# Kernel tuning notes

Hardware: AMD Instinct MI355X
Metric: run time of the kernel (lower is better)

## Reference

```python
import jax, jax.numpy as jnp
import numpy as np

B = 2048   # batch
C = 64     # EEG channels (num_eegch)
T = 125    # time samples -> pool5 -> 25 -> (p=5, 5)
H = 8      # num_heads
L = 6      # num_layers
D = 16     # num_projected_features
QK = 8     # qkv_len
P = 5      # tokens before cls
EPS = 1e-5


def setup_inputs() -> dict:
    key = jax.random.key(0)
    ks = iter(jax.random.split(key, 64))

    def nrm(shape, s=0.05):
        return jax.random.normal(next(ks), shape, jnp.float32) * s

    return {
        "x": jax.random.normal(next(ks), (B, 1, C, T), jnp.float32),
        "conv_t_w": nrm((8, 1, 1, 63)),
        "conv_t_b": nrm((8,)),
        "bn1_g": 1.0 + nrm((8,)),
        "bn1_b": nrm((8,)),
        "bn1_m": nrm((8,)),
        "bn1_v": 1.0 + 0.1 * jax.random.uniform(next(ks), (8,), jnp.float32),
        "conv_s_w": nrm((16, 1, C, 1)),
        "conv_s_b": nrm((16,)),
        "bn2_g": 1.0 + nrm((16,)),
        "bn2_b": nrm((16,)),
        "bn2_m": nrm((16,)),
        "bn2_v": 1.0 + 0.1 * jax.random.uniform(next(ks), (16,), jnp.float32),
        "proj_w": nrm((D, 16 * 5)),
        "proj_b": nrm((D,)),
        "cls_token": nrm((1, 1, D), 1.0),
        "pe": nrm((1, P + 1, D), 1.0),
        "qkv_w": nrm((L, 3 * H * QK, D)),
        "qkv_b": nrm((L, 3 * H * QK)),
        "out_w": nrm((L, D, H * QK)),
        "out_b": nrm((L, D)),
        "ln1_g": jnp.ones((L, D), jnp.float32),
        "ln1_b": jnp.zeros((L, D), jnp.float32),
        "ln2_g": jnp.ones((L, D), jnp.float32),
        "ln2_b": jnp.zeros((L, D), jnp.float32),
        "mlp_w1": nrm((L, 2 * D, D)),
        "mlp_b1": nrm((L, 2 * D)),
        "mlp_w2": nrm((L, D, 2 * D)),
        "mlp_b2": nrm((L, D)),
        "head_ln_g": jnp.ones((D,), jnp.float32),
        "head_ln_b": jnp.zeros((D,), jnp.float32),
        "head_w": nrm((2, D)),
        "head_b": nrm((2,)),
    }


def _bn(z, g, b, m, v):
    s = (g * jax.lax.rsqrt(v + EPS))[None, :, None, None]
    return (z - m[None, :, None, None]) * s + b[None, :, None, None]


def _ln(z, g, b):
    m = z.mean(-1, keepdims=True)
    var = jnp.mean((z - m) ** 2, -1, keepdims=True)
    return (z - m) * jax.lax.rsqrt(var + EPS) * g + b


def _forward(x, conv_t_w, conv_t_b, bn1_g, bn1_b, bn1_m, bn1_v,
             conv_s_w, conv_s_b, bn2_g, bn2_b, bn2_m, bn2_v,
             proj_w, proj_b, cls_token, pe,
             qkv_w, qkv_b, out_w, out_b, ln1_g, ln1_b, ln2_g, ln2_b,
             mlp_w1, mlp_b1, mlp_w2, mlp_b2,
             head_ln_g, head_ln_b, head_w, head_b):
    b = x.shape[0]
    dn = ('NCHW', 'OIHW', 'NCHW')
    # temporal conv, 'same' padding on width (kernel 63 -> pad 31/31)
    y = jax.lax.conv_general_dilated(x, conv_t_w, (1, 1), [(0, 0), (31, 31)], dimension_numbers=dn)
    y = _bn(y + conv_t_b[None, :, None, None], bn1_g, bn1_b, bn1_m, bn1_v)
    # grouped spatial conv collapses the EEG-channel axis
    y = jax.lax.conv_general_dilated(y, conv_s_w, (1, 1), 'VALID', dimension_numbers=dn, feature_group_count=8)
    y = _bn(y + conv_s_b[None, :, None, None], bn2_g, bn2_b, bn2_m, bn2_v)
    y = jax.nn.elu(y)                              # (b,16,1,125)
    y = y.reshape(b, 16, 1, T // 5, 5).mean(-1)    # avg_pool2d (1,5) -> (b,16,1,25)
    # dropout: identity at inference
    y = y.reshape(b, 16, 1, P, 5)
    y = jnp.swapaxes(y, 3, 4)
    tok = jnp.swapaxes(y.reshape(b, 16 * 5, P), 1, 2)   # (b,5,80)
    tok = tok @ proj_w.T + proj_b                       # (b,5,16)
    z = jnp.concatenate([jnp.broadcast_to(cls_token, (b, 1, D)), tok], axis=1) + pe  # (b,6,16)
    scale = QK ** -0.5
    for i in range(L):
        h1 = _ln(z, ln1_g[i], ln1_b[i])
        qkv = h1 @ qkv_w[i].T + qkv_b[i]                # (b,6,3*H*QK)
        q, k, v = jnp.split(qkv, 3, axis=-1)
        q = q.reshape(b, P + 1, H, QK).transpose(0, 2, 1, 3)
        k = k.reshape(b, P + 1, H, QK).transpose(0, 2, 1, 3)
        v = v.reshape(b, P + 1, H, QK).transpose(0, 2, 1, 3)
        att = jax.nn.softmax(jnp.einsum('bhsd,bhtd->bhst', q, k) * scale, axis=-1)
        o = jnp.einsum('bhst,bhtd->bhsd', att, v).transpose(0, 2, 1, 3).reshape(b, P + 1, H * QK)
        z = o @ out_w[i].T + out_b[i] + z
        h2 = _ln(z, ln2_g[i], ln2_b[i])
        m = jax.nn.gelu(h2 @ mlp_w1[i].T + mlp_b1[i], approximate=False) @ mlp_w2[i].T + mlp_b2[i]
        z = m + z
    cls = _ln(z[:, 0, :], head_ln_g, head_ln_b)
    return jax.nn.softmax(cls @ head_w.T + head_b, axis=-1)


def reference(x, conv_t_w, conv_t_b, bn1_g, bn1_b, bn1_m, bn1_v,
              conv_s_w, conv_s_b, bn2_g, bn2_b, bn2_m, bn2_v,
              proj_w, proj_b, cls_token, pe,
              qkv_w, qkv_b, out_w, out_b, ln1_g, ln1_b, ln2_g, ln2_b,
              mlp_w1, mlp_b1, mlp_w2, mlp_b2,
              head_ln_g, head_ln_b, head_w, head_b):
    return _forward(x, conv_t_w, conv_t_b, bn1_g, bn1_b, bn1_m, bn1_v,
                    conv_s_w, conv_s_b, bn2_g, bn2_b, bn2_m, bn2_v,
                    proj_w, proj_b, cls_token, pe,
                    qkv_w, qkv_b, out_w, out_b, ln1_g, ln1_b, ln2_g, ln2_b,
                    mlp_w1, mlp_b1, mlp_w2, mlp_b2,
                    head_ln_g, head_ln_b, head_w, head_b)
```

## Files before the change

### kernel.cpp

```cpp
#include <hip/hip_runtime.h>

#define WAVE_SYNC() do { asm volatile("" ::: "memory"); \
                         __builtin_amdgcn_wave_barrier(); \
                         asm volatile("" ::: "memory"); } while (0)

__device__ __forceinline__ float ln_norm16(float z, float g, float bb) {
    float s = z, q = z * z;
    #pragma unroll
    for (int off = 8; off >= 1; off >>= 1) {
        s += __shfl_xor(s, off, 16);
        q += __shfl_xor(q, off, 16);
    }
    float mean = s * 0.0625f;
    float var  = q * 0.0625f - mean * mean;
    return (z - mean) * rsqrtf(var + 1e-5f) * g + bb;
}

__device__ __forceinline__ float gelu_exact(float a) {
    float xa = fabsf(a) * 0.70710678118654752f;
    float tt = 1.f / (1.f + 0.3275911f * xa);
    float poly = tt * (0.254829592f + tt * (-0.284496736f + tt * (1.421413741f
               + tt * (-1.453152027f + tt * 1.061405429f))));
    float erfv = 1.f - poly * __expf(-xa * xa);
    erfv = a >= 0.f ? erfv : -erfv;
    return 0.5f * a * (1.f + erfv);
}

__device__ __forceinline__ float dot16(const float* h, float4 w0, float4 w1,
                                       float4 w2, float4 w3) {
    return h[0]*w0.x + h[1]*w0.y + h[2]*w0.z + h[3]*w0.w
         + h[4]*w1.x + h[5]*w1.y + h[6]*w1.z + h[7]*w1.w
         + h[8]*w2.x + h[9]*w2.y + h[10]*w2.z + h[11]*w2.w
         + h[12]*w3.x + h[13]*w3.y + h[14]*w3.z + h[15]*w3.w;
}

#define F_XS  0
#define F_PL  3168
#define F_TOT 3616

extern "C" __global__ __launch_bounds__(64, 2)
void eegnet_frontend(
    const float* __restrict__ x,
    const float* __restrict__ conv_t_w, const float* __restrict__ conv_t_b,
    const float* __restrict__ bn1_g, const float* __restrict__ bn1_b,
    const float* __restrict__ bn1_m, const float* __restrict__ bn1_v,
    const float* __restrict__ conv_s_w, const float* __restrict__ conv_s_b,
    const float* __restrict__ bn2_g, const float* __restrict__ bn2_b,
    const float* __restrict__ bn2_m, const float* __restrict__ bn2_v,
    const float* __restrict__ proj_w, const float* __restrict__ proj_b,
    float* __restrict__ tokws)
{
    __shared__ __align__(16) float sm[F_TOT];
    const int b    = blockIdx.x;
    const int lane = threadIdx.x;

    for (int i = lane; i < 16 * 73; i += 64) {
        int row = i / 73, k = i - row * 73;
        int off = (k < 32) ? k : (k + 125);
        sm[F_XS + row * 198 + off] = 0.f;
    }

    {
        const float* xb = x + (size_t)b * 8000;
        const int l2 = min(lane, 60);
        float a0[16], a1[16];
        #pragma unroll
        for (int o = 0; o < 16; ++o) { a0[o] = 0.f; a1[o] = 0.f; }
        #pragma unroll 16
        for (int c = 0; c < 64; ++c) {
            float xv0 = xb[c * 125 + lane];
            float xv1 = xb[c * 125 + 64 + l2];
            #pragma unroll
            for (int o = 0; o < 16; ++o) {
                float w = conv_s_w[o * 64 + c];
                a0[o] += w * xv0;
                a1[o] += w * xv1;
            }
        }
        #pragma unroll
        for (int o = 0; o < 16; ++o) {
            sm[F_XS + o * 198 + 32 + lane] = a0[o];
            if (lane < 61) sm[F_XS + o * 198 + 96 + lane] = a1[o];
        }
    }

    const int oo = lane & 15, qg = lane >> 4, gg = oo >> 1;
    float sa, cc;
    {
        float s1 = bn1_g[gg] * rsqrtf(bn1_v[gg] + 1e-5f);
        float b1 = (conv_t_b[gg] - bn1_m[gg]) * s1 + bn1_b[gg];
        float s2 = bn2_g[oo] * rsqrtf(bn2_v[oo] + 1e-5f);
        float ssum = 0.f;
        const float4* csw = reinterpret_cast<const float4*>(conv_s_w + oo * 64);
        #pragma unroll
        for (int i = 0; i < 16; ++i) {
            float4 v = csw[i];
            ssum += v.x + v.y + v.z + v.w;
        }
        sa = s1 * s2;
        cc = (b1 * ssum + conv_s_b[oo] - bn2_m[oo]) * s2 + bn2_b[oo];
    }
    float wt[63];
    #pragma unroll
    for (int k = 0; k < 63; ++k) wt[k] = conv_t_w[gg * 63 + k];

    WAVE_SYNC();

    #pragma unroll 1
    for (int jj = 0; jj < 7; ++jj) {
        int j  = qg * 7 + jj;
        int jc = min(j, 24);
        int base = F_XS + oo * 198 + 5 * jc + 1;
        float acc5[5] = {0.f, 0.f, 0.f, 0.f, 0.f};
        #pragma unroll
        for (int m = 0; m < 67; ++m) {
            float xv = sm[base + m];
            #pragma unroll
            for (int u = 0; u < 5; ++u)
                if (u <= m && m - u <= 62) acc5[u] += wt[m - u] * xv;
        }
        float psum = 0.f;
        #pragma unroll
        for (int u = 0; u < 5; ++u) {
            float v = acc5[u] * sa + cc;
            psum += (v > 0.f) ? v : (__expf(v) - 1.f);
        }
        if (j == jc) sm[F_PL + oo * 28 + j] = psum * 0.2f;
    }

    WAVE_SYNC();

    #pragma unroll
    for (int pass = 0; pass < 2; ++pass) {
        int oi = (pass == 0) ? lane : (64 + lane);
        int p = oi >> 4, dd = oi & 15;
        int pc = min(p, 4);
        bool act = (pass == 0) || (lane < 16);
        float acc = proj_b[dd];
        const float4* wp = reinterpret_cast<const float4*>(proj_w + dd * 80);
        #pragma unroll
        for (int i = 0; i < 20; ++i) {
            float4 w4 = wp[i];
            acc += w4.x * sm[F_PL + ((4*i+0)/5) * 28 + pc * 5 + ((4*i+0)%5)];
            acc += w4.y * sm[F_PL + ((4*i+1)/5) * 28 + pc * 5 + ((4*i+1)%5)];
            acc += w4.z * sm[F_PL + ((4*i+2)/5) * 28 + pc * 5 + ((4*i+2)%5)];
            acc += w4.w * sm[F_PL + ((4*i+3)/5) * 28 + pc * 5 + ((4*i+3)%5)];
        }
        if (act) tokws[b * 80 + pc * 16 + dd] = acc;
    }
}

#define WQKV 0
#define BQKV 3840
#define WOUT 4032
#define BOUT 5120
#define WM1  5136
#define BM1  5776
#define WM2  5808
#define BM2  6384
#define LN1G 6400
#define LN1B 6416
#define LN2G 6432
#define LN2B 6448
#define WEND 6464
#define SSTR 1568
#define SH1  0
#define SQKV 128
#define SMHS 1312
#define T_TOT (WEND + 4*SSTR)

extern "C" __global__ __launch_bounds__(256, 2)
void eegnet_transformer(
    const float* __restrict__ cls_token, const float* __restrict__ pe,
    const float* __restrict__ qkv_w, const float* __restrict__ qkv_b,
    const float* __restrict__ out_w, const float* __restrict__ out_b,
    const float* __restrict__ ln1_g, const float* __restrict__ ln1_b,
    const float* __restrict__ ln2_g, const float* __restrict__ ln2_b,
    const float* __restrict__ mlp_w1, const float* __restrict__ mlp_b1,
    const float* __restrict__ mlp_w2, const float* __restrict__ mlp_b2,
    const float* __restrict__ head_ln_g, const float* __restrict__ head_ln_b,
    const float* __restrict__ head_w, const float* __restrict__ head_b,
    const float* __restrict__ tokws, float* __restrict__ out)
{
    __shared__ __align__(16) float sm[T_TOT];
    const int tid = threadIdx.x;
    const int ss  = tid >> 7;
    const int u   = tid & 127;
    const int sA  = blockIdx.x * 4 + ss * 2;
    const int d16 = u & 15, qg = u >> 4;
    const int t6c = min(qg, 5);
    const int wav = u >> 6, al = u & 63;
    const int sbA = WEND + (ss * 2    ) * SSTR;
    const int sbB = WEND + (ss * 2 + 1) * SSTR;

    float zA, zB;
    {
        float peV = pe[t6c * 16 + d16];
        if (t6c == 0) {
            float cv = cls_token[d16];
            zA = cv + peV; zB = cv + peV;
        } else {
            zA = tokws[(sA    ) * 80 + (t6c - 1) * 16 + d16] + peV;
            zB = tokws[(sA + 1) * 80 + (t6c - 1) * 16 + d16] + peV;
        }
    }

    #pragma unroll 1
    for (int li = 0; li < 6; ++li) {
        __syncthreads();

        {
            const float4* s1 = reinterpret_cast<const float4*>(qkv_w + li * 3072);
            #pragma unroll
            for (int it = 0; it < 3; ++it) {
                int i = tid + it * 256;
                float4 v = s1[i];
                int j = i >> 2, k = (i & 3) << 2;
                *reinterpret_cast<float4*>(&sm[WQKV + j * 20 + k]) = v;
            }
            {
                float4 v = reinterpret_cast<const float4*>(out_w + li * 1024)[tid];
                int j = tid >> 4, k = (tid & 15) << 2;
                *reinterpret_cast<float4*>(&sm[WOUT + j * 68 + k]) = v;
            }
            if (tid < 128) {
                float4 v = reinterpret_cast<const float4*>(mlp_w1 + li * 512)[tid];
                int j = tid >> 2, k = (tid & 3) << 2;
                *reinterpret_cast<float4*>(&sm[WM1 + j * 20 + k]) = v;
            } else {
                int i = tid - 128;
                float4 v = reinterpret_cast<const float4*>(mlp_w2 + li * 512)[i];
                int j = i >> 3, k = (i & 7) << 2;
                *reinterpret_cast<float4*>(&sm[WM2 + j * 36 + k]) = v;
            }
            if (tid < 192) sm[BQKV + tid] = qkv_b[li * 192 + tid];
            else if (tid < 208) sm[BOUT + tid - 192] = out_b[li * 16 + tid - 192];
            else if (tid < 240) sm[BM1 + tid - 208]  = mlp_b1[li * 32 + tid - 208];
            else               sm[BM2 + tid - 240]  = mlp_b2[li * 16 + tid - 240];
            if (tid >= 64 && tid < 80)        sm[LN1G + tid - 64]  = ln1_g[li * 16 + tid - 64];
            else if (tid >= 80 && tid < 96)   sm[LN1B + tid - 80]  = ln1_b[li * 16 + tid - 80];
            else if (tid >= 96 && tid < 112)  sm[LN2G + tid - 96]  = ln2_g[li * 16 + tid - 96];
            else if (tid >= 112 && tid < 128) sm[LN2B + tid - 112] = ln2_b[li * 16 + tid - 112];
        }
        __syncthreads();

        {
            float g = sm[LN1G + d16], bb = sm[LN1B + d16];
            sm[sbA + SH1 + t6c * 20 + d16] = ln_norm16(zA, g, bb);
            sm[sbB + SH1 + t6c * 20 + d16] = ln_norm16(zB, g, bb);
        }
        WAVE_SYNC();

        float hrA[16], hrB[16];
        {
            const float4* pA = reinterpret_cast<const float4*>(&sm[sbA + SH1 + t6c * 20]);
            const float4* pB = reinterpret_cast<const float4*>(&sm[sbB + SH1 + t6c * 20]);
            #pragma unroll
            for (int i = 0; i < 4; ++i) {
                float4 va = pA[i], vb = pB[i];
                hrA[4*i+0]=va.x; hrA[4*i+1]=va.y; hrA[4*i+2]=va.z; hrA[4*i+3]=va.w;
                hrB[4*i+0]=vb.x; hrB[4*i+1]=vb.y; hrB[4*i+2]=vb.z; hrB[4*i+3]=vb.w;
            }
        }

        #pragma unroll 2
        for (int r = 0; r < 12; ++r) {
            int j = d16 + 16 * r;
            const float4* wp = reinterpret_cast<const float4*>(&sm[WQKV + j * 20]);
            float4 w0 = wp[0], w1_ = wp[1], w2_ = wp[2], w3_ = wp[3];
            float bb = sm[BQKV + j];
            sm[sbA + SQKV + t6c * 196 + j] = bb + dot16(hrA, w0, w1_, w2_, w3_);
            sm[sbB + SQKV + t6c * 196 + j] = bb + dot16(hrB, w0, w1_, w2_, w3_);
        }
        __syncthreads();

        {
            bool act = (wav == 0) ? (al < 32) : (al < 16);
            if (act) {
                int h  = al & 7;
                int qs = (wav == 0) ? (al >> 3) : 4 + (al >> 3);
                const int qoffA = sbA + SQKV + qs * 196 + h * 8;
                const int qoffB = sbB + SQKV + qs * 196 + h * 8;
                const float4* qpA = reinterpret_cast<const float4*>(&sm[qoffA]);
                const float4* qpB = reinterpret_cast<const float4*>(&sm[qoffB]);
                float4 qA0 = qpA[0], qA1 = qpA[1], qB0 = qpB[0], qB1 = qpB[1];
                float scA[6], scB[6];
                #pragma unroll
                for (int t = 0; t < 6; ++t) {
                    const float4* kA = reinterpret_cast<const float4*>(&sm[sbA + SQKV + t * 196 + 64 + h * 8]);
                    const float4* kB = reinterpret_cast<const float4*>(&sm[sbB + SQKV + t * 196 + 64 + h * 8]);
                    float4 a0 = kA[0], a1 = kA[1], b0 = kB[0], b1 = kB[1];
                    scA[t] = (qA0.x*a0.x + qA0.y*a0.y + qA0.z*a0.z + qA0.w*a0.w
                            + qA1.x*a1.x + qA1.y*a1.y + qA1.z*a1.z + qA1.w*a1.w)
                            * 0.35355339059327373f;
                    scB[t] = (qB0.x*b0.x + qB0.y*b0.y + qB0.z*b0.z + qB0.w*b0.w
                            + qB1.x*b1.x + qB1.y*b1.y + qB1.z*b1.z + qB1.w*b1.w)
                            * 0.35355339059327373f;
                }
                float mxA = scA[0], mxB = scB[0];
                #pragma unroll
                for (int t = 1; t < 6; ++t) { mxA = fmaxf(mxA, scA[t]); mxB = fmaxf(mxB, scB[t]); }
                float suA = 0.f, suB = 0.f;
                #pragma unroll
                for (int t = 0; t < 6; ++t) {
                    scA[t] = __expf(scA[t] - mxA); suA += scA[t];
                    scB[t] = __expf(scB[t] - mxB); suB += scB[t];
                }
                float ivA = 1.f / suA, ivB = 1.f / suB;
                float oA[8] = {0,0,0,0,0,0,0,0}, oB[8] = {0,0,0,0,0,0,0,0};
                #pragma unroll
                for (int t = 0; t < 6; ++t) {
                    const float4* vA = reinterpret_cast<const float4*>(&sm[sbA + SQKV + t * 196 + 128 + h * 8]);
                    const float4* vB = reinterpret_cast<const float4*>(&sm[sbB + SQKV + t * 196 + 128 + h * 8]);
                    float4 a0 = vA[0], a1 = vA[1], b0 = vB[0], b1 = vB[1];
                    float aa = scA[t] * ivA, ab = scB[t] * ivB;
                    oA[0]+=aa*a0.x; oA[1]+=aa*a0.y; oA[2]+=aa*a0.z; oA[3]+=aa*a0.w;
                    oA[4]+=aa*a1.x; oA[5]+=aa*a1.y; oA[6]+=aa*a1.z; oA[7]+=aa*a1.w;
                    oB[0]+=ab*b0.x; oB[1]+=ab*b0.y; oB[2]+=ab*b0.z; oB[3]+=ab*b0.w;
                    oB[4]+=ab*b1.x; oB[5]+=ab*b1.y; oB[6]+=ab*b1.z; oB[7]+=ab*b1.w;
                }
                *reinterpret_cast<float4*>(&sm[qoffA    ]) = float4{oA[0],oA[1],oA[2],oA[3]};
                *reinterpret_cast<float4*>(&sm[qoffA + 4]) = float4{oA[4],oA[5],oA[6],oA[7]};
                *reinterpret_cast<float4*>(&sm[qoffB    ]) = float4{oB[0],oB[1],oB[2],oB[3]};
                *reinterpret_cast<float4*>(&sm[qoffB + 4]) = float4{oB[4],oB[5],oB[6],oB[7]};
            }
        }
        WAVE_SYNC();

        {
            const float4* wop = reinterpret_cast<const float4*>(&sm[WOUT + d16 * 68]);
            const float4* oaA = reinterpret_cast<const float4*>(&sm[sbA + SQKV + t6c * 196]);
            const float4* oaB = reinterpret_cast<const float4*>(&sm[sbB + SQKV + t6c * 196]);
            float bb = sm[BOUT + d16];
            float aA = bb, aB = bb;
            #pragma unroll 4
            for (int i = 0; i < 16; ++i) {
                float4 w = wop[i];
                float4 va = oaA[i], vb = oaB[i];
                aA += va.x*w.x + va.y*w.y + va.z*w.z + va.w*w.w;
                aB += vb.x*w.x + vb.y*w.y + vb.z*w.z + vb.w*w.w;
            }
            zA += aA; zB += aB;
        }

        {
            float g = sm[LN2G + d16], bb = sm[LN2B + d16];
            sm[sbA + SH1 + t6c * 20 + d16] = ln_norm16(zA, g, bb);
            sm[sbB + SH1 + t6c * 20 + d16] = ln_norm16(zB, g, bb);
        }
        WAVE_SYNC();
        {
            const float4* pA = reinterpret_cast<const float4*>(&sm[sbA + SH1 + t6c * 20]);
            const float4* pB = reinterpret_cast<const float4*>(&sm[sbB + SH1 + t6c * 20]);
            #pragma unroll
            for (int i = 0; i < 4; ++i) {
                float4 va = pA[i], vb = pB[i];
                hrA[4*i+0]=va.x; hrA[4*i+1]=va.y; hrA[4*i+2]=va.z; hrA[4*i+3]=va.w;
                hrB[4*i+0]=vb.x; hrB[4*i+1]=vb.y; hrB[4*i+2]=vb.z; hrB[4*i+3]=vb.w;
            }
        }

        #pragma unroll
        for (int r = 0; r < 2; ++r) {
            int uu = d16 + 16 * r;
            const float4* wp = reinterpret_cast<const float4*>(&sm[WM1 + uu * 20]);
            float4 w0 = wp[0], w1_ = wp[1], w2_ = wp[2], w3_ = wp[3];
            float bb = sm[BM1 + uu];
            float aA = bb + dot16(hrA, w0, w1_, w2_, w3_);
            float aB = bb + dot16(hrB, w0, w1_, w2_, w3_);
            sm[sbA + SMHS + t6c * 36 + uu] = gelu_exact(aA);
            sm[sbB + SMHS + t6c * 36 + uu] = gelu_exact(aB);
        }
        WAVE_SYNC();

        {
            const float4* wp = reinterpret_cast<const float4*>(&sm[WM2 + d16 * 36]);
            const float4* mA = reinterpret_cast<const float4*>(&sm[sbA + SMHS + t6c * 36]);
            const float4* mB = reinterpret_cast<const float4*>(&sm[sbB + SMHS + t6c * 36]);
            float bb = sm[BM2 + d16];
            float aA = bb, aB = bb;
            #pragma unroll
            for (int i = 0; i < 8; ++i) {
                float4 w = wp[i];
                float4 va = mA[i], vb = mB[i];
                aA += va.x*w.x + va.y*w.y + va.z*w.z + va.w*w.w;
                aB += vb.x*w.x + vb.y*w.y + vb.z*w.z + vb.w*w.w;
            }
            zA += aA; zB += aB;
        }
    }

    if (u < 16) {
        float g = head_ln_g[d16], bb = head_ln_b[d16];
        float w0 = head_w[d16], w1 = head_w[16 + d16];
        float cvA = ln_norm16(zA, g, bb);
        float cvB = ln_norm16(zB, g, bb);
        float pA0 = cvA * w0, pA1 = cvA * w1;
        float pB0 = cvB * w0, pB1 = cvB * w1;
        #pragma unroll
        for (int off = 8; off >= 1; off >>= 1) {
            pA0 += __shfl_xor(pA0, off, 16);
            pA1 += __shfl_xor(pA1, off, 16);
            pB0 += __shfl_xor(pB0, off, 16);
            pB1 += __shfl_xor(pB1, off, 16);
        }
        if (u == 0) {
            float hb0 = head_b[0], hb1 = head_b[1];
            {
                float l0 = pA0 + hb0, l1 = pA1 + hb1;
                float mx = fmaxf(l0, l1);
                float e0 = __expf(l0 - mx), e1 = __expf(l1 - mx);
                float inv = 1.f / (e0 + e1);
                out[sA * 2 + 0] = e0 * inv;
                out[sA * 2 + 1] = e1 * inv;
            }
            {
                float l0 = pB0 + hb0, l1 = pB1 + hb1;
                float mx = fmaxf(l0, l1);
                float e0 = __expf(l0 - mx), e1 = __expf(l1 - mx);
                float inv = 1.f / (e0 + e1);
                out[(sA + 1) * 2 + 0] = e0 * inv;
                out[(sA + 1) * 2 + 1] = e1 * inv;
            }
        }
    }
}

extern "C" void kernel_launch(void* const* d_in, const int* in_sizes, int n_in,
                              void* d_out, int out_size, void* d_ws, size_t ws_size,
                              hipStream_t stream) {
    (void)n_in; (void)ws_size; (void)out_size;
    const float* a0  = (const float*)d_in[0];
    const float* a1  = (const float*)d_in[1];
    const float* a2  = (const float*)d_in[2];
    const float* a3  = (const float*)d_in[3];
    const float* a4  = (const float*)d_in[4];
    const float* a5  = (const float*)d_in[5];
    const float* a6  = (const float*)d_in[6];
    const float* a7  = (const float*)d_in[7];
    const float* a8  = (const float*)d_in[8];
    const float* a9  = (const float*)d_in[9];
    const float* a10 = (const float*)d_in[10];
    const float* a11 = (const float*)d_in[11];
    const float* a12 = (const float*)d_in[12];
    const float* a13 = (const float*)d_in[13];
    const float* a14 = (const float*)d_in[14];
    const float* a15 = (const float*)d_in[15];
    const float* a16 = (const float*)d_in[16];
    const float* a17 = (const float*)d_in[17];
    const float* a18 = (const float*)d_in[18];
    const float* a19 = (const float*)d_in[19];
    const float* a20 = (const float*)d_in[20];
    const float* a21 = (const float*)d_in[21];
    const float* a22 = (const float*)d_in[22];
    const float* a23 = (const float*)d_in[23];
    const float* a24 = (const float*)d_in[24];
    const float* a25 = (const float*)d_in[25];
    const float* a26 = (const float*)d_in[26];
    const float* a27 = (const float*)d_in[27];
    const float* a28 = (const float*)d_in[28];
    const float* a29 = (const float*)d_in[29];
    const float* a30 = (const float*)d_in[30];
    const float* a31 = (const float*)d_in[31];
    const float* a32 = (const float*)d_in[32];

    int Bn = in_sizes[0] / (64 * 125);
    float* tokws = (float*)d_ws;

    eegnet_frontend<<<Bn, 64, 0, stream>>>(
        a0, a1, a2, a3, a4, a5, a6, a7, a8, a9, a10, a11, a12, a13, a14, tokws);

    eegnet_transformer<<<Bn / 4, 256, 0, stream>>>(
        a15, a16, a17, a18, a19, a20, a21, a22, a23, a24, a25, a26, a27, a28,
        a29, a30, a31, a32, tokws, (float*)d_out);
}
```

Before: 233.0 us.

## Store transformer weights and activations in fp16 shared memory and use packed dot2

```diff
diff --git a/kernel.cpp b/kernel.cpp
--- a/kernel.cpp
+++ b/kernel.cpp
@@ -3,6 +3,37 @@
 #define WAVE_SYNC() do { asm volatile("" ::: "memory"); \
                          __builtin_amdgcn_wave_barrier(); \
                          asm volatile("" ::: "memory"); } while (0)
+
+typedef _Float16 h2 __attribute__((ext_vector_type(2)));
+typedef _Float16 h4 __attribute__((ext_vector_type(4)));
+typedef _Float16 h8 __attribute__((ext_vector_type(8)));
+
+__device__ __forceinline__ float fdot2(h2 a, h2 b, float c) {
+#if defined(__has_builtin)
+#if __has_builtin(__builtin_amdgcn_fdot2)
+    return __builtin_amdgcn_fdot2(a, b, c, false);
+#else
+    return (float)a[0]*(float)b[0] + (float)a[1]*(float)b[1] + c;
+#endif
+#else
+    return (float)a[0]*(float)b[0] + (float)a[1]*(float)b[1] + c;
+#endif
+}
+
+__device__ __forceinline__ float dot8h(h8 a, h8 b, float c) {
+    float s = c;
+    #pragma unroll
+    for (int i = 0; i < 4; ++i) {
+        h2 x = {a[2*i], a[2*i+1]};
+        h2 y = {b[2*i], b[2*i+1]};
+        s = fdot2(x, y, s);
+    }
+    return s;
+}
+
+__device__ __forceinline__ float dot16h(h8 a0, h8 a1, h8 b0, h8 b1, float c) {
+    return dot8h(a1, b1, dot8h(a0, b0, c));
+}
 
 __device__ __forceinline__ float ln_norm16(float z, float g, float bb) {
     float s = z, q = z * z;
@@ -24,14 +55,6 @@
     float erfv = 1.f - poly * __expf(-xa * xa);
     erfv = a >= 0.f ? erfv : -erfv;
     return 0.5f * a * (1.f + erfv);
-}
-
-__device__ __forceinline__ float dot16(const float* h, float4 w0, float4 w1,
-                                       float4 w2, float4 w3) {
-    return h[0]*w0.x + h[1]*w0.y + h[2]*w0.z + h[3]*w0.w
-         + h[4]*w1.x + h[5]*w1.y + h[6]*w1.z + h[7]*w1.w
-         + h[8]*w2.x + h[9]*w2.y + h[10]*w2.z + h[11]*w2.w
-         + h[12]*w3.x + h[13]*w3.y + h[14]*w3.z + h[15]*w3.w;
 }
 
 #define F_XS  0
@@ -106,7 +129,7 @@
 
     WAVE_SYNC();
 
-    #pragma unroll 1
+    #pragma unroll 2
     for (int jj = 0; jj < 7; ++jj) {
         int j  = qg * 7 + jj;
         int jc = min(j, 24);
@@ -150,24 +173,24 @@
     }
 }
 
-#define WQKV 0
-#define BQKV 3840
-#define WOUT 4032
-#define BOUT 5120
-#define WM1  5136
-#define BM1  5776
-#define WM2  5808
-#define BM2  6384
-#define LN1G 6400
-#define LN1B 6416
-#define LN2G 6432
-#define LN2B 6448
-#define WEND 6464
-#define SSTR 1568
-#define SH1  0
-#define SQKV 128
-#define SMHS 1312
-#define T_TOT (WEND + 4*SSTR)
+#define WQKVH 0
+#define WOUTH 4608
+#define WM1H  5760
+#define WM2H  6528
+#define BQKVF 3584
+#define BOUTF 3776
+#define BM1F  3792
+#define BM2F  3824
+#define LN1GF 3840
+#define LN1BF 3856
+#define LN2GF 3872
+#define LN2BF 3888
+#define SCR0  7808
+#define SSTRH 1584
+#define SH1H  0
+#define SQKVH 144
+#define SMHSH 1344
+#define T_BYTES 28288
 
 extern "C" __global__ __launch_bounds__(256, 2)
 void eegnet_transformer(
@@ -182,7 +205,10 @@
     const float* __restrict__ head_w, const float* __restrict__ head_b,
     const float* __restrict__ tokws, float* __restrict__ out)
 {
-    __shared__ __align__(16) float sm[T_TOT];
+    __shared__ __align__(16) unsigned char smb[T_BYTES];
+    float*    smf = reinterpret_cast<float*>(smb);
+    _Float16* smh = reinterpret_cast<_Float16*>(smb);
+
     const int tid = threadIdx.x;
     const int ss  = tid >> 7;
     const int u   = tid & 127;
@@ -190,8 +216,8 @@
     const int d16 = u & 15, qg = u >> 4;
     const int t6c = min(qg, 5);
     const int wav = u >> 6, al = u & 63;
-    const int sbA = WEND + (ss * 2    ) * SSTR;
-    const int sbB = WEND + (ss * 2 + 1) * SSTR;
+    const int sbA = SCR0 + (ss * 2    ) * SSTRH;
+    const int sbB = SCR0 + (ss * 2 + 1) * SSTRH;
 
     float zA, zB;
     {
@@ -216,61 +242,58 @@
                 int i = tid + it * 256;
                 float4 v = s1[i];
                 int j = i >> 2, k = (i & 3) << 2;
-                *reinterpret_cast<float4*>(&sm[WQKV + j * 20 + k]) = v;
+                h4 hv = {(_Float16)v.x, (_Float16)v.y, (_Float16)v.z, (_Float16)v.w};
+                *reinterpret_cast<h4*>(&smh[WQKVH + j * 24 + k]) = hv;
             }
             {
                 float4 v = reinterpret_cast<const float4*>(out_w + li * 1024)[tid];
                 int j = tid >> 4, k = (tid & 15) << 2;
-                *reinterpret_cast<float4*>(&sm[WOUT + j * 68 + k]) = v;
+                h4 hv = {(_Float16)v.x, (_Float16)v.y, (_Float16)v.z, (_Float16)v.w};
+                *reinterpret_cast<h4*>(&smh[WOUTH + j * 72 + k]) = hv;
             }
             if (tid < 128) {
                 float4 v = reinterpret_cast<const float4*>(mlp_w1 + li * 512)[tid];
                 int j = tid >> 2, k = (tid & 3) << 2;
-                *reinterpret_cast<float4*>(&sm[WM1 + j * 20 + k]) = v;
+                h4 hv = {(_Float16)v.x, (_Float16)v.y, (_Float16)v.z, (_Float16)v.w};
+                *reinterpret_cast<h4*>(&smh[WM1H + j * 24 + k]) = hv;
             } else {
                 int i = tid - 128;
                 float4 v = reinterpret_cast<const float4*>(mlp_w2 + li * 512)[i];
                 int j = i >> 3, k = (i & 7) << 2;
-                *reinterpret_cast<float4*>(&sm[WM2 + j * 36 + k]) = v;
-            }
-            if (tid < 192) sm[BQKV + tid] = qkv_b[li * 192 + tid];
-            else if (tid < 208) sm[BOUT + tid - 192] = out_b[li * 16 + tid - 192];
-            else if (tid < 240) sm[BM1 + tid - 208]  = mlp_b1[li * 32 + tid - 208];
-            else               sm[BM2 + tid - 240]  = mlp_b2[li * 16 + tid - 240];
-            if (tid >= 64 && tid < 80)        sm[LN1G + tid - 64]  = ln1_g[li * 16 + tid - 64];
-            else if (tid >= 80 && tid < 96)   sm[LN1B + tid - 80]  = ln1_b[li * 16 + tid - 80];
-            else if (tid >= 96 && tid < 112)  sm[LN2G + tid - 96]  = ln2_g[li * 16 + tid - 96];
-            else if (tid >= 112 && tid < 128) sm[LN2B + tid - 112] = ln2_b[li * 16 + tid - 112];
+                h4 hv = {(_Float16)v.x, (_Float16)v.y, (_Float16)v.z, (_Float16)v.w};
+                *reinterpret_cast<h4*>(&smh[WM2H + j * 40 + k]) = hv;
+            }
+            if (tid < 192) smf[BQKVF + tid] = qkv_b[li * 192 + tid];
+            else if (tid < 208) smf[BOUTF + tid - 192] = out_b[li * 16 + tid - 192];
+            else if (tid < 240) smf[BM1F + tid - 208]  = mlp_b1[li * 32 + tid - 208];
+            else               smf[BM2F + tid - 240]  = mlp_b2[li * 16 + tid - 240];
+            if (tid >= 64 && tid < 80)        smf[LN1GF + tid - 64]  = ln1_g[li * 16 + tid - 64];
+            else if (tid >= 80 && tid < 96)   smf[LN1BF + tid - 80]  = ln1_b[li * 16 + tid - 80];
+            else if (tid >= 96 && tid < 112)  smf[LN2GF + tid - 96]  = ln2_g[li * 16 + tid - 96];
+            else if (tid >= 112 && tid < 128) smf[LN2BF + tid - 112] = ln2_b[li * 16 + tid - 112];
         }
         __syncthreads();
 
         {
-            float g = sm[LN1G + d16], bb = sm[LN1B + d16];
-            sm[sbA + SH1 + t6c * 20 + d16] = ln_norm16(zA, g, bb);
-            sm[sbB + SH1 + t6c * 20 + d16] = ln_norm16(zB, g, bb);
+            float g = smf[LN1GF + d16], bb = smf[LN1BF + d16];
+            smh[sbA + SH1H + t6c * 24 + d16] = (_Float16)ln_norm16(zA, g, bb);
+            smh[sbB + SH1H + t6c * 24 + d16] = (_Float16)ln_norm16(zB, g, bb);
         }
         WAVE_SYNC();
 
-        float hrA[16], hrB[16];
-        {
-            const float4* pA = reinterpret_cast<const float4*>(&sm[sbA + SH1 + t6c * 20]);
-            const float4* pB = reinterpret_cast<const float4*>(&sm[sbB + SH1 + t6c * 20]);
-            #pragma unroll
-            for (int i = 0; i < 4; ++i) {
-                float4 va = pA[i], vb = pB[i];
-                hrA[4*i+0]=va.x; hrA[4*i+1]=va.y; hrA[4*i+2]=va.z; hrA[4*i+3]=va.w;
-                hrB[4*i+0]=vb.x; hrB[4*i+1]=vb.y; hrB[4*i+2]=vb.z; hrB[4*i+3]=vb.w;
-            }
-        }
+        h8 hA0 = *reinterpret_cast<const h8*>(&smh[sbA + SH1H + t6c * 24]);
+        h8 hA1 = *reinterpret_cast<const h8*>(&smh[sbA + SH1H + t6c * 24 + 8]);
+        h8 hB0 = *reinterpret_cast<const h8*>(&smh[sbB + SH1H + t6c * 24]);
+        h8 hB1 = *reinterpret_cast<const h8*>(&smh[sbB + SH1H + t6c * 24 + 8]);
 
         #pragma unroll 2
         for (int r = 0; r < 12; ++r) {
             int j = d16 + 16 * r;
-            const float4* wp = reinterpret_cast<const float4*>(&sm[WQKV + j * 20]);
-            float4 w0 = wp[0], w1_ = wp[1], w2_ = wp[2], w3_ = wp[3];
-            float bb = sm[BQKV + j];
-            sm[sbA + SQKV + t6c * 196 + j] = bb + dot16(hrA, w0, w1_, w2_, w3_);
-            sm[sbB + SQKV + t6c * 196 + j] = bb + dot16(hrB, w0, w1_, w2_, w3_);
+            h8 w0 = *reinterpret_cast<const h8*>(&smh[WQKVH + j * 24]);
+            h8 w1 = *reinterpret_cast<const h8*>(&smh[WQKVH + j * 24 + 8]);
+            float bb = smf[BQKVF + j];
+            smh[sbA + SQKVH + t6c * 200 + j] = (_Float16)dot16h(hA0, hA1, w0, w1, bb);
+            smh[sbB + SQKVH + t6c * 200 + j] = (_Float16)dot16h(hB0, hB1, w0, w1, bb);
         }
         __syncthreads();
 
@@ -279,23 +302,17 @@
             if (act) {
                 int h  = al & 7;
                 int qs = (wav == 0) ? (al >> 3) : 4 + (al >> 3);
-                const int qoffA = sbA + SQKV + qs * 196 + h * 8;
-                const int qoffB = sbB + SQKV + qs * 196 + h * 8;
-                const float4* qpA = reinterpret_cast<const float4*>(&sm[qoffA]);
-                const float4* qpB = reinterpret_cast<const float4*>(&sm[qoffB]);
-                float4 qA0 = qpA[0], qA1 = qpA[1], qB0 = qpB[0], qB1 = qpB[1];
+                const int qoffA = sbA + SQKVH + qs * 200 + h * 8;
+                const int qoffB = sbB + SQKVH + qs * 200 + h * 8;
+                h8 qA = *reinterpret_cast<const h8*>(&smh[qoffA]);
+                h8 qB = *reinterpret_cast<const h8*>(&smh[qoffB]);
                 float scA[6], scB[6];
                 #pragma unroll
                 for (int t = 0; t < 6; ++t) {
-                    const float4* kA = reinterpret_cast<const float4*>(&sm[sbA + SQKV + t * 196 + 64 + h * 8]);
-                    const float4* kB = reinterpret_cast<const float4*>(&sm[sbB + SQKV + t * 196 + 64 + h * 8]);
-                    float4 a0 = kA[0], a1 = kA[1], b0 = kB[0], b1 = kB[1];
-                    scA[t] = (qA0.x*a0.x + qA0.y*a0.y + qA0.z*a0.z + qA0.w*a0.w
-                            + qA1.x*a1.x + qA1.y*a1.y + qA1.z*a1.z + qA1.w*a1.w)
-                            * 0.35355339059327373f;
-                    scB[t] = (qB0.x*b0.x + qB0.y*b0.y + qB0.z*b0.z + qB0.w*b0.w
-                            + qB1.x*b1.x + qB1.y*b1.y + qB1.z*b1.z + qB1.w*b1.w)
-                            * 0.35355339059327373f;
+                    h8 kA = *reinterpret_cast<const h8*>(&smh[sbA + SQKVH + t * 200 + 64 + h * 8]);
+                    h8 kB = *reinterpret_cast<const h8*>(&smh[sbB + SQKVH + t * 200 + 64 + h * 8]);
+                    scA[t] = dot8h(qA, kA, 0.f) * 0.35355339059327373f;
+                    scB[t] = dot8h(qB, kB, 0.f) * 0.35355339059327373f;
                 }
                 float mxA = scA[0], mxB = scB[0];
                 #pragma unroll
@@ -307,84 +324,82 @@
                     scB[t] = __expf(scB[t] - mxB); suB += scB[t];
                 }
                 float ivA = 1.f / suA, ivB = 1.f / suB;
-                float oA[8] = {0,0,0,0,0,0,0,0}, oB[8] = {0,0,0,0,0,0,0,0};
+                h2 oA[4], oB[4];
+                #pragma unroll
+                for (int k2 = 0; k2 < 4; ++k2) { oA[k2] = h2{0, 0}; oB[k2] = h2{0, 0}; }
                 #pragma unroll
                 for (int t = 0; t < 6; ++t) {
-                    const float4* vA = reinterpret_cast<const float4*>(&sm[sbA + SQKV + t * 196 + 128 + h * 8]);
-                    const float4* vB = reinterpret_cast<const float4*>(&sm[sbB + SQKV + t * 196 + 128 + h * 8]);
-                    float4 a0 = vA[0], a1 = vA[1], b0 = vB[0], b1 = vB[1];
-                    float aa = scA[t] * ivA, ab = scB[t] * ivB;
-                    oA[0]+=aa*a0.x; oA[1]+=aa*a0.y; oA[2]+=aa*a0.z; oA[3]+=aa*a0.w;
-                    oA[4]+=aa*a1.x; oA[5]+=aa*a1.y; oA[6]+=aa*a1.z; oA[7]+=aa*a1.w;
-                    oB[0]+=ab*b0.x; oB[1]+=ab*b0.y; oB[2]+=ab*b0.z; oB[3]+=ab*b0.w;
-                    oB[4]+=ab*b1.x; oB[5]+=ab*b1.y; oB[6]+=ab*b1.z; oB[7]+=ab*b1.w;
+                    h8 vA = *reinterpret_cast<const h8*>(&smh[sbA + SQKVH + t * 200 + 128 + h * 8]);
+                    h8 vB = *reinterpret_cast<const h8*>(&smh[sbB + SQKVH + t * 200 + 128 + h * 8]);
+                    _Float16 aa = (_Float16)(scA[t] * ivA);
+                    _Float16 ab = (_Float16)(scB[t] * ivB);
+                    h2 av = {aa, aa}, bv = {ab, ab};
+                    #pragma unroll
+                    for (int k2 = 0; k2 < 4; ++k2) {
+                        h2 va = {vA[2*k2], vA[2*k2+1]};
+                        h2 vb = {vB[2*k2], vB[2*k2+1]};
+                        oA[k2] += av * va;
+                        oB[k2] += bv * vb;
+                    }
                 }
-                *reinterpret_cast<float4*>(&sm[qoffA    ]) = float4{oA[0],oA[1],oA[2],oA[3]};
-                *reinterpret_cast<float4*>(&sm[qoffA + 4]) = float4{oA[4],oA[5],oA[6],oA[7]};
-                *reinterpret_cast<float4*>(&sm[qoffB    ]) = float4{oB[0],oB[1],oB[2],oB[3]};
-                *reinterpret_cast<float4*>(&sm[qoffB + 4]) = float4{oB[4],oB[5],oB[6],oB[7]};
+                h8 stA, stB;
+                #pragma unroll
+                for (int k2 = 0; k2 < 4; ++k2) {
+                    stA[2*k2] = oA[k2][0]; stA[2*k2+1] = oA[k2][1];
+                    stB[2*k2] = oB[k2][0]; stB[2*k2+1] = oB[k2][1];
+                }
+                *reinterpret_cast<h8*>(&smh[qoffA]) = stA;
+                *reinterpret_cast<h8*>(&smh[qoffB]) = stB;
             }
         }
         WAVE_SYNC();
 
         {
-            const float4* wop = reinterpret_cast<const float4*>(&sm[WOUT + d16 * 68]);
-            const float4* oaA = reinterpret_cast<const float4*>(&sm[sbA + SQKV + t6c * 196]);
-            const float4* oaB = reinterpret_cast<const float4*>(&sm[sbB + SQKV + t6c * 196]);
-            float bb = sm[BOUT + d16];
-            float aA = bb, aB = bb;
-            #pragma unroll 4
-            for (int i = 0; i < 16; ++i) {
-                float4 w = wop[i];
-                float4 va = oaA[i], vb = oaB[i];
-                aA += va.x*w.x + va.y*w.y + va.z*w.z + va.w*w.w;
-                aB += vb.x*w.x + vb.y*w.y + vb.z*w.z + vb.w*w.w;
+            float aA = smf[BOUTF + d16], aB = aA;
+            #pragma unroll
+            for (int i = 0; i < 8; ++i) {
+                h8 w  = *reinterpret_cast<const h8*>(&smh[WOUTH + d16 * 72 + 8 * i]);
+                h8 va = *reinterpret_cast<const h8*>(&smh[sbA + SQKVH + t6c * 200 + 8 * i]);
+                h8 vb = *reinterpret_cast<const h8*>(&smh[sbB + SQKVH + t6c * 200 + 8 * i]);
+                aA = dot8h(va, w, aA);
+                aB = dot8h(vb, w, aB);
             }
             zA += aA; zB += aB;
         }
 
         {
-            float g = sm[LN2G + d16], bb = sm[LN2B + d16];
-            sm[sbA + SH1 + t6c * 20 + d16] = ln_norm16(zA, g, bb);
-            sm[sbB + SH1 + t6c * 20 + d16] = ln_norm16(zB, g, bb);
+            float g = smf[LN2GF + d16], bb = smf[LN2BF + d16];
+            smh[sbA + SH1H + t6c * 24 + d16] = (_Float16)ln_norm16(zA, g, bb);
+            smh[sbB + SH1H + t6c * 24 + d16] = (_Float16)ln_norm16(zB, g, bb);
         }
         WAVE_SYNC();
-        {
-            const float4* pA = reinterpret_cast<const float4*>(&sm[sbA + SH1 + t6c * 20]);
-            const float4* pB = reinterpret_cast<const float4*>(&sm[sbB + SH1 + t6c * 20]);
+        hA0 = *reinterpret_cast<const h8*>(&smh[sbA + SH1H + t6c * 24]);
+        hA1 = *reinterpret_cast<const h8*>(&smh[sbA + SH1H + t6c * 24 + 8]);
+        hB0 = *reinterpret_cast<const h8*>(&smh[sbB + SH1H + t6c * 24]);
+        hB1 = *reinterpret_cast<const h8*>(&smh[sbB + SH1H + t6c * 24 + 8]);
+
+        #pragma unroll
+        for (int r = 0; r < 2; ++r) {
+            int uu = d16 + 16 * r;
+            h8 w0 = *reinterpret_cast<const h8*>(&smh[WM1H + uu * 24]);
+            h8 w1 = *reinterpret_cast<const h8*>(&smh[WM1H + uu * 24 + 8]);
+            float bb = smf[BM1F + uu];
+            float aA = dot16h(hA0, hA1, w0, w1, bb);
+            float aB = dot16h(hB0, hB1, w0, w1, bb);
+            smh[sbA + SMHSH + t6c * 40 + uu] = (_Float16)gelu_exact(aA);
+            smh[sbB + SMHSH + t6c * 40 + uu] = (_Float16)gelu_exact(aB);
+        }
+        WAVE_SYNC();
+
+        {
+            float aA = smf[BM2F + d16], aB = aA;
             #pragma unroll
             for (int i = 0; i < 4; ++i) {
-                float4 va = pA[i], vb = pB[i];
-                hrA[4*i+0]=va.x; hrA[4*i+1]=va.y; hrA[4*i+2]=va.z; hrA[4*i+3]=va.w;
-                hrB[4*i+0]=vb.x; hrB[4*i+1]=vb.y; hrB[4*i+2]=vb.z; hrB[4*i+3]=vb.w;
-            }
-        }
-
-        #pragma unroll
-        for (int r = 0; r < 2; ++r) {
-            int uu = d16 + 16 * r;
-            const float4* wp = reinterpret_cast<const float4*>(&sm[WM1 + uu * 20]);
-            float4 w0 = wp[0], w1_ = wp[1], w2_ = wp[2], w3_ = wp[3];
-            float bb = sm[BM1 + uu];
-            float aA = bb + dot16(hrA, w0, w1_, w2_, w3_);
-            float aB = bb + dot16(hrB, w0, w1_, w2_, w3_);
-            sm[sbA + SMHS + t6c * 36 + uu] = gelu_exact(aA);
-            sm[sbB + SMHS + t6c * 36 + uu] = gelu_exact(aB);
-        }
-        WAVE_SYNC();
-
-        {
-            const float4* wp = reinterpret_cast<const float4*>(&sm[WM2 + d16 * 36]);
-            const float4* mA = reinterpret_cast<const float4*>(&sm[sbA + SMHS + t6c * 36]);
-            const float4* mB = reinterpret_cast<const float4*>(&sm[sbB + SMHS + t6c * 36]);
-            float bb = sm[BM2 + d16];
-            float aA = bb, aB = bb;
-            #pragma unroll
-            for (int i = 0; i < 8; ++i) {
-                float4 w = wp[i];
-                float4 va = mA[i], vb = mB[i];
-                aA += va.x*w.x + va.y*w.y + va.z*w.z + va.w*w.w;
-                aB += vb.x*w.x + vb.y*w.y + vb.z*w.z + vb.w*w.w;
+                h8 w  = *reinterpret_cast<const h8*>(&smh[WM2H + d16 * 40 + 8 * i]);
+                h8 va = *reinterpret_cast<const h8*>(&smh[sbA + SMHSH + t6c * 40 + 8 * i]);
+                h8 vb = *reinterpret_cast<const h8*>(&smh[sbB + SMHSH + t6c * 40 + 8 * i]);
+                aA = dot8h(va, w, aA);
+                aB = dot8h(vb, w, aB);
             }
             zA += aA; zB += aB;
         }
```

Result: faster. 216.8 us (-6.9%).
